# Kernel optimization log

Measured on AMD Instinct MI355X. Metric: run time of the kernel, lower is better.

Reference implementation:

```python
import jax, jax.numpy as jnp
import numpy as np

EPS = 1e-06
H = 25  # num heads


def _rmsnorm(x, w, eps=EPS):
    # normalize over last dim in float32, as in the torch module
    xf = x.astype(jnp.float32)
    var = jnp.mean(xf * xf, axis=-1, keepdims=True)
    return (w * (xf * jax.lax.rsqrt(var + eps))).astype(x.dtype)


def setup_inputs() -> dict:
    key = jax.random.key(0)
    ks = jax.random.split(key, 4)
    B, N, C = 8, 1025, 3200
    x = jax.random.normal(ks[0], (B, N, C), dtype=jnp.float32)
    qkv_w = jax.random.normal(ks[1], (C, 3 * C), dtype=jnp.float32) * (C ** -0.5)
    qkv_b = jnp.zeros((3 * C,), dtype=jnp.float32)
    q_norm_w = jnp.ones((C,), dtype=jnp.float32)
    k_norm_w = jnp.ones((C,), dtype=jnp.float32)
    proj_w = jax.random.normal(ks[2], (C, C), dtype=jnp.float32) * (C ** -0.5)
    proj_b = jnp.zeros((C,), dtype=jnp.float32)
    return {"x": x, "qkv_w": qkv_w, "qkv_b": qkv_b, "q_norm_w": q_norm_w,
            "k_norm_w": k_norm_w, "proj_w": proj_w, "proj_b": proj_b}


def reference(x, qkv_w, qkv_b, q_norm_w, k_norm_w, proj_w, proj_b):
    B, N, C = x.shape
    D = C // H
    scale = D ** -0.5
    qkv = x @ qkv_w + qkv_b                      # [B, N, 3C]
    q, k, v = jnp.split(qkv, 3, axis=-1)         # each [B, N, C]
    # QK RMSNorm is over the FULL embed_dim (heads flattened), per source.
    q = _rmsnorm(q, q_norm_w)
    k = _rmsnorm(k, k_norm_w)
    q = q.reshape(B, N, H, D)
    k = k.reshape(B, N, H, D)
    v = v.reshape(B, N, H, D)
    attn = jnp.einsum('bqhd,bkhd->bhqk', q * scale, k)   # [B, H, N, N]
    attn = jax.nn.softmax(attn, axis=-1)
    out = jnp.einsum('bhqk,bkhd->bqhd', attn, v).reshape(B, N, C)
    return out @ proj_w + proj_b
```

## Files before the change

kernel.cpp:

```cpp
#include <hip/hip_runtime.h>
#include <hip/hip_bf16.h>
#include <math.h>

#define B_ 8
#define N_ 1025
#define C_ 3200
#define H_ 25
#define D_ 128
#define M_ (B_ * N_)
#define C3_ (3 * C_)

typedef unsigned short u16;
typedef unsigned int u32;
typedef short bf16x8 __attribute__((ext_vector_type(8)));
typedef float f32x4 __attribute__((ext_vector_type(4)));

__device__ inline void load_lds16(const void* g, void* s) {
    __builtin_amdgcn_global_load_lds(
        (const __attribute__((address_space(1))) void*)g,
        (__attribute__((address_space(3))) void*)s, 16, 0, 0);
}

__device__ inline void split_pair(float x0, float x1, u32& hpk, u32& lpk) {
    __hip_bfloat162 h2 = __float22bfloat162_rn(float2{x0, x1});
    union { __hip_bfloat162 b; u32 u; } cv; cv.b = h2;
    u32 h = cv.u;
    float hf0 = __uint_as_float(h << 16);
    float hf1 = __uint_as_float(h & 0xFFFF0000u);
    __hip_bfloat162 l2 = __float22bfloat162_rn(float2{x0 - hf0, x1 - hf1});
    union { __hip_bfloat162 b; u32 u; } cl; cl.b = l2;
    hpk = h; lpk = cl.u;
}

__device__ inline void split1(float x, u16& h, u16& l) {
    union { __hip_bfloat16 b; u16 u; } ch, cl;
    ch.b = __float2bfloat16(x);
    float hf = __uint_as_float(((u32)ch.u) << 16);
    cl.b = __float2bfloat16(x - hf);
    h = ch.u; l = cl.u;
}

__global__ __launch_bounds__(256) void convert_tsplit(
    const float* __restrict__ in, u16* __restrict__ hi, u16* __restrict__ lo,
    int K, int Nn, int strideN)
{
    __shared__ float T[32][33];
    const int tid = threadIdx.x;
    const int nb = blockIdx.x * 32, kb = blockIdx.y * 32;
    #pragma unroll
    for (int p = 0; p < 4; ++p) {
        int k = p * 8 + (tid >> 5), n = tid & 31;
        T[k][n] = in[(size_t)(kb + k) * strideN + nb + n];
    }
    __syncthreads();
    const int nn = tid >> 3, k0 = (tid & 7) * 4;
    u32 h0, l0, h1, l1;
    split_pair(T[k0][nn], T[k0 + 1][nn], h0, l0);
    split_pair(T[k0 + 2][nn], T[k0 + 3][nn], h1, l1);
    size_t o = (size_t)(nb + nn) * K + kb + k0;
    *(uint2*)&hi[o] = make_uint2(h0, h1);
    *(uint2*)&lo[o] = make_uint2(l0, l1);
}

__global__ __launch_bounds__(256) void gemm_asplit(
    const float* __restrict__ A,
    const u16* __restrict__ Bh, const u16* __restrict__ Bl,
    const float* __restrict__ bias, float* __restrict__ Cc,
    int M, int N, int ldc)
{
    __shared__ u16 As_h[2][512][8];
    __shared__ u16 As_l[2][512][8];
    __shared__ u16 Bs_h[2][512][8];
    __shared__ u16 Bs_l[2][512][8];

    const int tid  = threadIdx.x;
    const int lane = tid & 63;
    const int w    = tid >> 6;
    const int wm   = w & 1, wn = w >> 1;
    const int lr = lane & 15, lg = lane >> 4;

    const int gX   = gridDim.x;
    const int nwg  = gX * gridDim.y;
    const int orig = blockIdx.y * gX + blockIdx.x;
    const int q8 = nwg >> 3, r8 = nwg & 7;
    const int xcd = orig & 7, oi = orig >> 3;
    const int wg = (xcd < r8 ? xcd * (q8 + 1)
                             : r8 * (q8 + 1) + (xcd - r8) * q8) + oi;
    const int rowBase = (wg / gX) * 128;
    const int colBase = (wg % gX) * 128;

    const int brow = tid & 127, bkc = tid >> 7;
    const size_t boff0 = (size_t)(colBase + brow) * C_ + bkc * 8;
    const size_t boff1 = (size_t)(colBase + brow) * C_ + (bkc + 2) * 8;
    const int ldsA = (w * 64) * 8;
    const int ldsB = (256 + w * 64) * 8;

    const int arow = tid >> 1;
    const int akh  = (tid & 1) * 16;
    const int kc0  = akh >> 3;
    int gr0 = rowBase + arow; if (gr0 >= M) gr0 = M - 1;
    const float* aptr = A + (size_t)gr0 * C_ + akh;

    auto STAGE_B = [&](int bb, int k0) {
        const int bo = bb * 512 * 8;
        load_lds16(Bh + boff0 + k0, (u16*)Bs_h + bo + ldsA);
        load_lds16(Bl + boff0 + k0, (u16*)Bs_l + bo + ldsA);
        load_lds16(Bh + boff1 + k0, (u16*)Bs_h + bo + ldsB);
        load_lds16(Bl + boff1 + k0, (u16*)Bs_l + bo + ldsB);
    };

    auto ASPLIT = [&](int bb, const float4& x0, const float4& x1,
                      const float4& x2, const float4& x3) {
        u32 h0,h1,h2,h3,h4,h5,h6,h7, l0,l1,l2,l3,l4,l5,l6,l7;
        split_pair(x0.x, x0.y, h0, l0); split_pair(x0.z, x0.w, h1, l1);
        split_pair(x1.x, x1.y, h2, l2); split_pair(x1.z, x1.w, h3, l3);
        split_pair(x2.x, x2.y, h4, l4); split_pair(x2.z, x2.w, h5, l5);
        split_pair(x3.x, x3.y, h6, l6); split_pair(x3.z, x3.w, h7, l7);
        *(uint4*)&As_h[bb][kc0 * 128 + arow][0]       = make_uint4(h0,h1,h2,h3);
        *(uint4*)&As_h[bb][(kc0 + 1) * 128 + arow][0] = make_uint4(h4,h5,h6,h7);
        *(uint4*)&As_l[bb][kc0 * 128 + arow][0]       = make_uint4(l0,l1,l2,l3);
        *(uint4*)&As_l[bb][(kc0 + 1) * 128 + arow][0] = make_uint4(l4,l5,l6,l7);
    };

    f32x4 acc[4][4] = {};
    float4 a0, a1, a2, a3;

    {
        float4 p0 = *(const float4*)(aptr + 0);
        float4 p1 = *(const float4*)(aptr + 4);
        float4 p2 = *(const float4*)(aptr + 8);
        float4 p3 = *(const float4*)(aptr + 12);
        ASPLIT(0, p0, p1, p2, p3);
    }
    STAGE_B(0, 0);
    {
        const float* ap = aptr + 32;
        a0 = *(const float4*)(ap + 0);
        a1 = *(const float4*)(ap + 4);
        a2 = *(const float4*)(ap + 8);
        a3 = *(const float4*)(ap + 12);
    }
    asm volatile("s_waitcnt vmcnt(0) lgkmcnt(0)" ::: "memory");
    __builtin_amdgcn_s_barrier();
    asm volatile("" ::: "memory");

    int cur = 0;
    for (int k0 = 0; k0 < C_; k0 += 32) {
        if (k0 + 32 < C_) {
            STAGE_B(cur ^ 1, k0 + 32);
            ASPLIT(cur ^ 1, a0, a1, a2, a3);
            if (k0 + 64 < C_) {
                const float* ap = aptr + k0 + 64;
                a0 = *(const float4*)(ap + 0);
                a1 = *(const float4*)(ap + 4);
                a2 = *(const float4*)(ap + 8);
                a3 = *(const float4*)(ap + 12);
            }
            asm volatile("s_waitcnt vmcnt(8)" ::: "memory");
        } else {
            asm volatile("s_waitcnt vmcnt(0)" ::: "memory");
        }
        asm volatile("s_waitcnt lgkmcnt(0)" ::: "memory");
        __builtin_amdgcn_s_barrier();
        asm volatile("" ::: "memory");

        bf16x8 ah[4], al[4], bh[4], bl[4];
        #pragma unroll
        for (int i = 0; i < 4; ++i) {
            ah[i] = *(const bf16x8*)&As_h[cur][lg * 128 + wm * 64 + i * 16 + lr][0];
            al[i] = *(const bf16x8*)&As_l[cur][lg * 128 + wm * 64 + i * 16 + lr][0];
            bh[i] = *(const bf16x8*)&Bs_h[cur][lg * 128 + wn * 64 + i * 16 + lr][0];
            bl[i] = *(const bf16x8*)&Bs_l[cur][lg * 128 + wn * 64 + i * 16 + lr][0];
        }
        #pragma unroll
        for (int j = 0; j < 4; ++j)
            #pragma unroll
            for (int i = 0; i < 4; ++i)
                acc[i][j] = __builtin_amdgcn_mfma_f32_16x16x32_bf16(
                    ah[i], bh[j], acc[i][j], 0, 0, 0);
        #pragma unroll
        for (int j = 0; j < 4; ++j)
            #pragma unroll
            for (int i = 0; i < 4; ++i)
                acc[i][j] = __builtin_amdgcn_mfma_f32_16x16x32_bf16(
                    al[i], bh[j], acc[i][j], 0, 0, 0);
        #pragma unroll
        for (int j = 0; j < 4; ++j)
            #pragma unroll
            for (int i = 0; i < 4; ++i)
                acc[i][j] = __builtin_amdgcn_mfma_f32_16x16x32_bf16(
                    ah[i], bl[j], acc[i][j], 0, 0, 0);

        asm volatile("s_waitcnt lgkmcnt(0)" ::: "memory");
        __builtin_amdgcn_s_barrier();
        asm volatile("" ::: "memory");
        cur ^= 1;
    }

    #pragma unroll
    for (int i = 0; i < 4; ++i) {
        #pragma unroll
        for (int j = 0; j < 4; ++j) {
            int gc = colBase + wn * 64 + j * 16 + lr;
            float bv = bias[gc];
            #pragma unroll
            for (int r = 0; r < 4; ++r) {
                int gr = rowBase + wm * 64 + i * 16 + lg * 4 + r;
                if (gr < M) Cc[(size_t)gr * ldc + gc] = acc[i][j][r] + bv;
            }
        }
    }
}

__global__ __launch_bounds__(256) void gemm_bf16split(
    const u16* __restrict__ Ah, const u16* __restrict__ Al,
    const u16* __restrict__ Bh, const u16* __restrict__ Bl,
    const float* __restrict__ bias, float* __restrict__ Cc,
    int M, int N, int ldc)
{
    __shared__ u16 As_h[2][512][8];
    __shared__ u16 As_l[2][512][8];
    __shared__ u16 Bs_h[2][512][8];
    __shared__ u16 Bs_l[2][512][8];

    const int tid  = threadIdx.x;
    const int lane = tid & 63;
    const int w    = tid >> 6;
    const int wm   = w & 1, wn = w >> 1;
    const int lr = lane & 15, lg = lane >> 4;

    const int gX   = gridDim.x;
    const int nwg  = gX * gridDim.y;
    const int orig = blockIdx.y * gX + blockIdx.x;
    const int q8 = nwg >> 3, r8 = nwg & 7;
    const int xcd = orig & 7, oi = orig >> 3;
    const int wg = (xcd < r8 ? xcd * (q8 + 1)
                             : r8 * (q8 + 1) + (xcd - r8) * q8) + oi;
    const int rowBase = (wg / gX) * 128;
    const int colBase = (wg % gX) * 128;

    const int row = tid & 127, kc = tid >> 7;
    int ar = rowBase + row; if (ar >= M) ar = M - 1;
    const size_t aoff0 = (size_t)ar * C_ + kc * 8;
    const size_t aoff1 = (size_t)ar * C_ + (kc + 2) * 8;
    const size_t boff0 = (size_t)(colBase + row) * C_ + kc * 8;
    const size_t boff1 = (size_t)(colBase + row) * C_ + (kc + 2) * 8;
    const int ldsA = (w * 64) * 8;
    const int ldsB = (256 + w * 64) * 8;

    auto STAGE = [&](int bb, int k0) {
        const int bo = bb * 512 * 8;
        load_lds16(Ah + aoff0 + k0, (u16*)As_h + bo + ldsA);
        load_lds16(Al + aoff0 + k0, (u16*)As_l + bo + ldsA);
        load_lds16(Bh + boff0 + k0, (u16*)Bs_h + bo + ldsA);
        load_lds16(Bl + boff0 + k0, (u16*)Bs_l + bo + ldsA);
        load_lds16(Ah + aoff1 + k0, (u16*)As_h + bo + ldsB);
        load_lds16(Al + aoff1 + k0, (u16*)As_l + bo + ldsB);
        load_lds16(Bh + boff1 + k0, (u16*)Bs_h + bo + ldsB);
        load_lds16(Bl + boff1 + k0, (u16*)Bs_l + bo + ldsB);
    };

    f32x4 acc[4][4] = {};

    STAGE(0, 0);
    int cur = 0;
    for (int k0 = 0; k0 < C_; k0 += 32) {
        if (k0 + 32 < C_) {
            STAGE(cur ^ 1, k0 + 32);
            asm volatile("s_waitcnt vmcnt(8)" ::: "memory");
        } else {
            asm volatile("s_waitcnt vmcnt(0)" ::: "memory");
        }
        __builtin_amdgcn_s_barrier();
        asm volatile("" ::: "memory");

        bf16x8 ah[4], al[4], bh[4], bl[4];
        #pragma unroll
        for (int i = 0; i < 4; ++i) {
            ah[i] = *(const bf16x8*)&As_h[cur][lg * 128 + wm * 64 + i * 16 + lr][0];
            al[i] = *(const bf16x8*)&As_l[cur][lg * 128 + wm * 64 + i * 16 + lr][0];
            bh[i] = *(const bf16x8*)&Bs_h[cur][lg * 128 + wn * 64 + i * 16 + lr][0];
            bl[i] = *(const bf16x8*)&Bs_l[cur][lg * 128 + wn * 64 + i * 16 + lr][0];
        }
        #pragma unroll
        for (int j = 0; j < 4; ++j)
            #pragma unroll
            for (int i = 0; i < 4; ++i)
                acc[i][j] = __builtin_amdgcn_mfma_f32_16x16x32_bf16(
                    ah[i], bh[j], acc[i][j], 0, 0, 0);
        #pragma unroll
        for (int j = 0; j < 4; ++j)
            #pragma unroll
            for (int i = 0; i < 4; ++i)
                acc[i][j] = __builtin_amdgcn_mfma_f32_16x16x32_bf16(
                    al[i], bh[j], acc[i][j], 0, 0, 0);
        #pragma unroll
        for (int j = 0; j < 4; ++j)
            #pragma unroll
            for (int i = 0; i < 4; ++i)
                acc[i][j] = __builtin_amdgcn_mfma_f32_16x16x32_bf16(
                    ah[i], bl[j], acc[i][j], 0, 0, 0);

        asm volatile("s_waitcnt lgkmcnt(0)" ::: "memory");
        __builtin_amdgcn_s_barrier();
        asm volatile("" ::: "memory");
        cur ^= 1;
    }

    #pragma unroll
    for (int i = 0; i < 4; ++i) {
        #pragma unroll
        for (int j = 0; j < 4; ++j) {
            int gc = colBase + wn * 64 + j * 16 + lr;
            float bv = bias[gc];
            #pragma unroll
            for (int r = 0; r < 4; ++r) {
                int gr = rowBase + wm * 64 + i * 16 + lg * 4 + r;
                if (gr < M) Cc[(size_t)gr * ldc + gc] = acc[i][j][r] + bv;
            }
        }
    }
}

__global__ __launch_bounds__(256) void rmsnorm_kernel(
    float* __restrict__ qkv, const float* __restrict__ qw,
    const float* __restrict__ kw)
{
    const int row   = blockIdx.x >> 1;
    const int which = blockIdx.x & 1;
    float* p = qkv + (size_t)row * C3_ + which * C_;
    const float* w = which ? kw : qw;
    const int tid = threadIdx.x;

    float ss = 0.f;
    for (int i = tid; i < C_ / 4; i += 256) {
        float4 v = ((const float4*)p)[i];
        ss += v.x * v.x + v.y * v.y + v.z * v.z + v.w * v.w;
    }
    #pragma unroll
    for (int off = 32; off; off >>= 1) ss += __shfl_down(ss, off);

    __shared__ float wsum[4];
    __shared__ float stot;
    if ((tid & 63) == 0) wsum[tid >> 6] = ss;
    __syncthreads();
    if (tid == 0) stot = wsum[0] + wsum[1] + wsum[2] + wsum[3];
    __syncthreads();

    const float scale = rsqrtf(stot / (float)C_ + 1e-6f);
    for (int i = tid; i < C_ / 4; i += 256) {
        float4 v  = ((const float4*)p)[i];
        float4 wv = ((const float4*)w)[i];
        v.x *= scale * wv.x; v.y *= scale * wv.y;
        v.z *= scale * wv.z; v.w *= scale * wv.w;
        ((float4*)p)[i] = v;
    }
}

__global__ __launch_bounds__(256, 2) void flash_mfma(
    const float* __restrict__ qkv, u16* __restrict__ aoh, u16* __restrict__ aol)
{
    __shared__ u16 Kh[4][32][32];
    __shared__ u16 Kl[4][32][32];
    __shared__ u16 Vth[128][40];
    __shared__ u16 Vtl[128][40];
    __shared__ u16 Ph[4][16][40];
    __shared__ u16 Pl[4][16][40];

    const int b   = blockIdx.z;
    const int h   = blockIdx.y;
    const int q0  = blockIdx.x * 64;
    const int tid = threadIdx.x;
    const int lane = tid & 63;
    const int w    = tid >> 6;
    const int lr = lane & 15, lg = lane >> 4;
    const float scale = 0.088388347648318447f;

    bf16x8 qh[4], ql[4];
    {
        int qr = q0 + w * 16 + lr;
        if (qr >= N_) qr = N_ - 1;
        const float* qp = qkv + (size_t)(b * N_ + qr) * C3_ + h * D_;
        #pragma unroll
        for (int c = 0; c < 4; ++c) {
            float4 x0 = *(const float4*)(qp + c * 32 + lg * 8);
            float4 x1 = *(const float4*)(qp + c * 32 + lg * 8 + 4);
            union { u32 u[4]; bf16x8 v; } Hq, Lq;
            split_pair(x0.x * scale, x0.y * scale, Hq.u[0], Lq.u[0]);
            split_pair(x0.z * scale, x0.w * scale, Hq.u[1], Lq.u[1]);
            split_pair(x1.x * scale, x1.y * scale, Hq.u[2], Lq.u[2]);
            split_pair(x1.z * scale, x1.w * scale, Hq.u[3], Lq.u[3]);
            qh[c] = Hq.v; ql[c] = Lq.v;
        }
    }

    const float* Kbase = qkv + (size_t)b * N_ * C3_ + C_ + h * D_;
    const float* Vbase = qkv + (size_t)b * N_ * C3_ + 2 * C_ + h * D_;

    const int skr = tid >> 3;
    const int skd = (tid & 7) * 16;
    const int svk = (tid & 15) * 2;
    const int svd = (tid >> 4) * 4;

    float4 kg[4], vg[2][2];

    auto stage_load = [&](int kt) {
        int kk = kt * 32 + skr;
        if (kk < N_) {
            const float* p = Kbase + (size_t)kk * C3_ + skd;
            kg[0] = *(const float4*)(p + 0);
            kg[1] = *(const float4*)(p + 4);
            kg[2] = *(const float4*)(p + 8);
            kg[3] = *(const float4*)(p + 12);
        } else {
            kg[0] = kg[1] = kg[2] = kg[3] = make_float4(0.f, 0.f, 0.f, 0.f);
        }
        #pragma unroll
        for (int r = 0; r < 2; ++r) {
            int vk = kt * 32 + svk + r;
            if (vk < N_) {
                const float* p = Vbase + (size_t)vk * C3_ + svd;
                vg[0][r] = *(const float4*)(p);
                vg[1][r] = *(const float4*)(p + 64);
            } else {
                vg[0][r] = make_float4(0.f, 0.f, 0.f, 0.f);
                vg[1][r] = make_float4(0.f, 0.f, 0.f, 0.f);
            }
        }
    };

    auto stage_store = [&]() {
        #pragma unroll
        for (int i = 0; i < 4; ++i) {
            int d = skd + i * 4;
            int c = d >> 5, dd = d & 31;
            u32 h0, l0, h1, l1;
            split_pair(kg[i].x, kg[i].y, h0, l0);
            split_pair(kg[i].z, kg[i].w, h1, l1);
            *(uint2*)&Kh[c][skr][dd] = make_uint2(h0, h1);
            *(uint2*)&Kl[c][skr][dd] = make_uint2(l0, l1);
        }
        #pragma unroll
        for (int half = 0; half < 2; ++half) {
            float a0[4] = { vg[half][0].x, vg[half][0].y, vg[half][0].z, vg[half][0].w };
            float a1[4] = { vg[half][1].x, vg[half][1].y, vg[half][1].z, vg[half][1].w };
            #pragma unroll
            for (int i = 0; i < 4; ++i) {
                int d = svd + half * 64 + i;
                u32 hp, lp;
                split_pair(a0[i], a1[i], hp, lp);
                *(u32*)&Vth[d][svk] = hp;
                *(u32*)&Vtl[d][svk] = lp;
            }
        }
    };

    f32x4 oacc[8] = {};
    float m[4]    = { -INFINITY, -INFINITY, -INFINITY, -INFINITY };
    float lsum[4] = { 0.f, 0.f, 0.f, 0.f };

    const int nkt = (N_ + 31) / 32;
    stage_load(0);
    for (int kt = 0; kt < nkt; ++kt) {
        __syncthreads();
        stage_store();
        __syncthreads();
        if (kt + 1 < nkt) stage_load(kt + 1);

        f32x4 s0 = {}, s1 = {};
        #pragma unroll
        for (int c = 0; c < 4; ++c) {
            bf16x8 kh0 = *(const bf16x8*)&Kh[c][lr][lg * 8];
            bf16x8 kl0 = *(const bf16x8*)&Kl[c][lr][lg * 8];
            bf16x8 kh1 = *(const bf16x8*)&Kh[c][16 + lr][lg * 8];
            bf16x8 kl1 = *(const bf16x8*)&Kl[c][16 + lr][lg * 8];
            s0 = __builtin_amdgcn_mfma_f32_16x16x32_bf16(qh[c], kh0, s0, 0, 0, 0);
            s0 = __builtin_amdgcn_mfma_f32_16x16x32_bf16(ql[c], kh0, s0, 0, 0, 0);
            s0 = __builtin_amdgcn_mfma_f32_16x16x32_bf16(qh[c], kl0, s0, 0, 0, 0);
            s1 = __builtin_amdgcn_mfma_f32_16x16x32_bf16(qh[c], kh1, s1, 0, 0, 0);
            s1 = __builtin_amdgcn_mfma_f32_16x16x32_bf16(ql[c], kh1, s1, 0, 0, 0);
            s1 = __builtin_amdgcn_mfma_f32_16x16x32_bf16(qh[c], kl1, s1, 0, 0, 0);
        }

        const int kb = kt * 32;
        const bool v0 = (kb + lr) < N_;
        const bool v1 = (kb + 16 + lr) < N_;
        #pragma unroll
        for (int r = 0; r < 4; ++r) {
            if (!v0) s0[r] = -INFINITY;
            if (!v1) s1[r] = -INFINITY;
        }

        #pragma unroll
        for (int r = 0; r < 4; ++r) {
            float mt = fmaxf(s0[r], s1[r]);
            mt = fmaxf(mt, __shfl_xor(mt, 1));
            mt = fmaxf(mt, __shfl_xor(mt, 2));
            mt = fmaxf(mt, __shfl_xor(mt, 4));
            mt = fmaxf(mt, __shfl_xor(mt, 8));
            float mn = fmaxf(m[r], mt);
            float al = __expf(m[r] - mn);
            m[r] = mn;
            float p0 = __expf(s0[r] - mn);
            float p1 = __expf(s1[r] - mn);
            float ls = p0 + p1;
            ls += __shfl_xor(ls, 1);
            ls += __shfl_xor(ls, 2);
            ls += __shfl_xor(ls, 4);
            ls += __shfl_xor(ls, 8);
            lsum[r] = lsum[r] * al + ls;
            #pragma unroll
            for (int dt = 0; dt < 8; ++dt) oacc[dt][r] *= al;

            u16 hh, ll;
            split1(p0, hh, ll);
            Ph[w][lg * 4 + r][lr] = hh;
            Pl[w][lg * 4 + r][lr] = ll;
            split1(p1, hh, ll);
            Ph[w][lg * 4 + r][16 + lr] = hh;
            Pl[w][lg * 4 + r][16 + lr] = ll;
        }

        bf16x8 pah = *(const bf16x8*)&Ph[w][lr][lg * 8];
        bf16x8 pal = *(const bf16x8*)&Pl[w][lr][lg * 8];
        #pragma unroll
        for (int dt = 0; dt < 8; ++dt) {
            bf16x8 vh = *(const bf16x8*)&Vth[dt * 16 + lr][lg * 8];
            bf16x8 vl = *(const bf16x8*)&Vtl[dt * 16 + lr][lg * 8];
            oacc[dt] = __builtin_amdgcn_mfma_f32_16x16x32_bf16(pah, vh, oacc[dt], 0, 0, 0);
            oacc[dt] = __builtin_amdgcn_mfma_f32_16x16x32_bf16(pal, vh, oacc[dt], 0, 0, 0);
            oacc[dt] = __builtin_amdgcn_mfma_f32_16x16x32_bf16(pah, vl, oacc[dt], 0, 0, 0);
        }
    }

    #pragma unroll
    for (int r = 0; r < 4; ++r) {
        int q = q0 + w * 16 + lg * 4 + r;
        if (q < N_) {
            float inv = 1.f / lsum[r];
            size_t base = (size_t)(b * N_ + q) * C_ + h * D_ + lr;
            #pragma unroll
            for (int dt = 0; dt < 8; ++dt) {
                u16 hh, ll;
                split1(oacc[dt][r] * inv, hh, ll);
                aoh[base + dt * 16] = hh;
                aol[base + dt * 16] = ll;
            }
        }
    }
}

extern "C" void kernel_launch(void* const* d_in, const int* in_sizes, int n_in,
                              void* d_out, int out_size, void* d_ws, size_t ws_size,
                              hipStream_t stream)
{
    const float* x        = (const float*)d_in[0];
    const float* qkv_w    = (const float*)d_in[1];
    const float* qkv_b    = (const float*)d_in[2];
    const float* q_norm_w = (const float*)d_in[3];
    const float* k_norm_w = (const float*)d_in[4];
    const float* proj_w   = (const float*)d_in[5];
    const float* proj_b   = (const float*)d_in[6];
    float* out = (float*)d_out;

    const size_t fQ = (size_t)M_ * C3_;
    const size_t fA = (size_t)M_ * C_;
    const size_t wC = (size_t)C_ * C_;

    float* qkv = (float*)d_ws;
    u16*   R   = (u16*)(qkv + fQ);

    dim3 blk(256);

    u16* wh = R;
    u16* wl = wh + wC;
    for (int j = 0; j < 3; ++j) {
        convert_tsplit<<<dim3(C_ / 32, C_ / 32), blk, 0, stream>>>(
            qkv_w + (size_t)j * C_, wh, wl, C_, C_, C3_);
        gemm_asplit<<<dim3(C_ / 128, (M_ + 127) / 128), blk, 0, stream>>>(
            x, wh, wl, qkv_b + j * C_, qkv + (size_t)j * C_, M_, C_, C3_);
    }

    rmsnorm_kernel<<<dim3(M_ * 2), blk, 0, stream>>>(qkv, q_norm_w, k_norm_w);
    u16* aoh = R;
    u16* aol = R + fA;
    flash_mfma<<<dim3((N_ + 63) / 64, H_, B_), blk, 0, stream>>>(qkv, aoh, aol);

    u16* ph = (u16*)d_ws;
    u16* pl = ph + wC;
    convert_tsplit<<<dim3(C_ / 32, C_ / 32), blk, 0, stream>>>(
        proj_w, ph, pl, C_, C_, C_);
    gemm_bf16split<<<dim3(C_ / 128, (M_ + 127) / 128), blk, 0, stream>>>(
        aoh, aol, ph, pl, proj_b, out, M_, C_, C_);
}
```

Before: 4.507 ms.

## Reuse asplit GEMM for projection, restructure barriers, add MFMA priority

The attention kernel now writes fp32 output directly instead of pre-split bf16 hi/lo arrays. The output projection runs through the gemm_asplit kernel, which splits A on the fly, and the separate gemm_bf16split kernel is removed. In gemm_asplit, the wait and barrier move to the top of each iteration, one end-of-loop barrier is dropped, and s_setprio is raised around the MFMA block. This removes the extra bf16 split-array traffic and one sync per step, but attention now writes more bytes in fp32, and the new barrier placement risks a race on the double buffer.

```diff
diff --git a/kernel.cpp b/kernel.cpp
--- a/kernel.cpp
+++ b/kernel.cpp
@@ -140,12 +140,13 @@
         a2 = *(const float4*)(ap + 8);
         a3 = *(const float4*)(ap + 12);
     }
-    asm volatile("s_waitcnt vmcnt(0) lgkmcnt(0)" ::: "memory");
-    __builtin_amdgcn_s_barrier();
-    asm volatile("" ::: "memory");
 
     int cur = 0;
     for (int k0 = 0; k0 < C_; k0 += 32) {
+        asm volatile("s_waitcnt vmcnt(0) lgkmcnt(0)" ::: "memory");
+        __builtin_amdgcn_s_barrier();
+        asm volatile("" ::: "memory");
+
         if (k0 + 32 < C_) {
             STAGE_B(cur ^ 1, k0 + 32);
             ASPLIT(cur ^ 1, a0, a1, a2, a3);
@@ -156,13 +157,7 @@
                 a2 = *(const float4*)(ap + 8);
                 a3 = *(const float4*)(ap + 12);
             }
-            asm volatile("s_waitcnt vmcnt(8)" ::: "memory");
-        } else {
-            asm volatile("s_waitcnt vmcnt(0)" ::: "memory");
-        }
-        asm volatile("s_waitcnt lgkmcnt(0)" ::: "memory");
-        __builtin_amdgcn_s_barrier();
-        asm volatile("" ::: "memory");
+        }
 
         bf16x8 ah[4], al[4], bh[4], bl[4];
         #pragma unroll
@@ -172,6 +167,7 @@
             bh[i] = *(const bf16x8*)&Bs_h[cur][lg * 128 + wn * 64 + i * 16 + lr][0];
             bl[i] = *(const bf16x8*)&Bs_l[cur][lg * 128 + wn * 64 + i * 16 + lr][0];
         }
+        __builtin_amdgcn_s_setprio(1);
         #pragma unroll
         for (int j = 0; j < 4; ++j)
             #pragma unroll
@@ -190,120 +186,7 @@
             for (int i = 0; i < 4; ++i)
                 acc[i][j] = __builtin_amdgcn_mfma_f32_16x16x32_bf16(
                     ah[i], bl[j], acc[i][j], 0, 0, 0);
-
-        asm volatile("s_waitcnt lgkmcnt(0)" ::: "memory");
-        __builtin_amdgcn_s_barrier();
-        asm volatile("" ::: "memory");
-        cur ^= 1;
-    }
-
-    #pragma unroll
-    for (int i = 0; i < 4; ++i) {
-        #pragma unroll
-        for (int j = 0; j < 4; ++j) {
-            int gc = colBase + wn * 64 + j * 16 + lr;
-            float bv = bias[gc];
-            #pragma unroll
-            for (int r = 0; r < 4; ++r) {
-                int gr = rowBase + wm * 64 + i * 16 + lg * 4 + r;
-                if (gr < M) Cc[(size_t)gr * ldc + gc] = acc[i][j][r] + bv;
-            }
-        }
-    }
-}
-
-__global__ __launch_bounds__(256) void gemm_bf16split(
-    const u16* __restrict__ Ah, const u16* __restrict__ Al,
-    const u16* __restrict__ Bh, const u16* __restrict__ Bl,
-    const float* __restrict__ bias, float* __restrict__ Cc,
-    int M, int N, int ldc)
-{
-    __shared__ u16 As_h[2][512][8];
-    __shared__ u16 As_l[2][512][8];
-    __shared__ u16 Bs_h[2][512][8];
-    __shared__ u16 Bs_l[2][512][8];
-
-    const int tid  = threadIdx.x;
-    const int lane = tid & 63;
-    const int w    = tid >> 6;
-    const int wm   = w & 1, wn = w >> 1;
-    const int lr = lane & 15, lg = lane >> 4;
-
-    const int gX   = gridDim.x;
-    const int nwg  = gX * gridDim.y;
-    const int orig = blockIdx.y * gX + blockIdx.x;
-    const int q8 = nwg >> 3, r8 = nwg & 7;
-    const int xcd = orig & 7, oi = orig >> 3;
-    const int wg = (xcd < r8 ? xcd * (q8 + 1)
-                             : r8 * (q8 + 1) + (xcd - r8) * q8) + oi;
-    const int rowBase = (wg / gX) * 128;
-    const int colBase = (wg % gX) * 128;
-
-    const int row = tid & 127, kc = tid >> 7;
-    int ar = rowBase + row; if (ar >= M) ar = M - 1;
-    const size_t aoff0 = (size_t)ar * C_ + kc * 8;
-    const size_t aoff1 = (size_t)ar * C_ + (kc + 2) * 8;
-    const size_t boff0 = (size_t)(colBase + row) * C_ + kc * 8;
-    const size_t boff1 = (size_t)(colBase + row) * C_ + (kc + 2) * 8;
-    const int ldsA = (w * 64) * 8;
-    const int ldsB = (256 + w * 64) * 8;
-
-    auto STAGE = [&](int bb, int k0) {
-        const int bo = bb * 512 * 8;
-        load_lds16(Ah + aoff0 + k0, (u16*)As_h + bo + ldsA);
-        load_lds16(Al + aoff0 + k0, (u16*)As_l + bo + ldsA);
-        load_lds16(Bh + boff0 + k0, (u16*)Bs_h + bo + ldsA);
-        load_lds16(Bl + boff0 + k0, (u16*)Bs_l + bo + ldsA);
-        load_lds16(Ah + aoff1 + k0, (u16*)As_h + bo + ldsB);
-        load_lds16(Al + aoff1 + k0, (u16*)As_l + bo + ldsB);
-        load_lds16(Bh + boff1 + k0, (u16*)Bs_h + bo + ldsB);
-        load_lds16(Bl + boff1 + k0, (u16*)Bs_l + bo + ldsB);
-    };
-
-    f32x4 acc[4][4] = {};
-
-    STAGE(0, 0);
-    int cur = 0;
-    for (int k0 = 0; k0 < C_; k0 += 32) {
-        if (k0 + 32 < C_) {
-            STAGE(cur ^ 1, k0 + 32);
-            asm volatile("s_waitcnt vmcnt(8)" ::: "memory");
-        } else {
-            asm volatile("s_waitcnt vmcnt(0)" ::: "memory");
-        }
-        __builtin_amdgcn_s_barrier();
-        asm volatile("" ::: "memory");
-
-        bf16x8 ah[4], al[4], bh[4], bl[4];
-        #pragma unroll
-        for (int i = 0; i < 4; ++i) {
-            ah[i] = *(const bf16x8*)&As_h[cur][lg * 128 + wm * 64 + i * 16 + lr][0];
-            al[i] = *(const bf16x8*)&As_l[cur][lg * 128 + wm * 64 + i * 16 + lr][0];
-            bh[i] = *(const bf16x8*)&Bs_h[cur][lg * 128 + wn * 64 + i * 16 + lr][0];
-            bl[i] = *(const bf16x8*)&Bs_l[cur][lg * 128 + wn * 64 + i * 16 + lr][0];
-        }
-        #pragma unroll
-        for (int j = 0; j < 4; ++j)
-            #pragma unroll
-            for (int i = 0; i < 4; ++i)
-                acc[i][j] = __builtin_amdgcn_mfma_f32_16x16x32_bf16(
-                    ah[i], bh[j], acc[i][j], 0, 0, 0);
-        #pragma unroll
-        for (int j = 0; j < 4; ++j)
-            #pragma unroll
-            for (int i = 0; i < 4; ++i)
-                acc[i][j] = __builtin_amdgcn_mfma_f32_16x16x32_bf16(
-                    al[i], bh[j], acc[i][j], 0, 0, 0);
-        #pragma unroll
-        for (int j = 0; j < 4; ++j)
-            #pragma unroll
-            for (int i = 0; i < 4; ++i)
-                acc[i][j] = __builtin_amdgcn_mfma_f32_16x16x32_bf16(
-                    ah[i], bl[j], acc[i][j], 0, 0, 0);
-
-        asm volatile("s_waitcnt lgkmcnt(0)" ::: "memory");
-        __builtin_amdgcn_s_barrier();
-        asm volatile("" ::: "memory");
+        __builtin_amdgcn_s_setprio(0);
         cur ^= 1;
     }
 
@@ -358,7 +241,7 @@
 }
 
 __global__ __launch_bounds__(256, 2) void flash_mfma(
-    const float* __restrict__ qkv, u16* __restrict__ aoh, u16* __restrict__ aol)
+    const float* __restrict__ qkv, float* __restrict__ attn_out)
 {
     __shared__ u16 Kh[4][32][32];
     __shared__ u16 Kl[4][32][32];
@@ -538,14 +421,9 @@
         int q = q0 + w * 16 + lg * 4 + r;
         if (q < N_) {
             float inv = 1.f / lsum[r];
-            size_t base = (size_t)(b * N_ + q) * C_ + h * D_ + lr;
-            #pragma unroll
-            for (int dt = 0; dt < 8; ++dt) {
-                u16 hh, ll;
-                split1(oacc[dt][r] * inv, hh, ll);
-                aoh[base + dt * 16] = hh;
-                aol[base + dt * 16] = ll;
-            }
+            float* op = attn_out + (size_t)(b * N_ + q) * C_ + h * D_ + lr;
+            #pragma unroll
+            for (int dt = 0; dt < 8; ++dt) op[dt * 16] = oacc[dt][r] * inv;
         }
     }
 }
@@ -582,14 +460,13 @@
     }
 
     rmsnorm_kernel<<<dim3(M_ * 2), blk, 0, stream>>>(qkv, q_norm_w, k_norm_w);
-    u16* aoh = R;
-    u16* aol = R + fA;
-    flash_mfma<<<dim3((N_ + 63) / 64, H_, B_), blk, 0, stream>>>(qkv, aoh, aol);
+    float* attn_out = (float*)R;
+    flash_mfma<<<dim3((N_ + 63) / 64, H_, B_), blk, 0, stream>>>(qkv, attn_out);
 
     u16* ph = (u16*)d_ws;
     u16* pl = ph + wC;
     convert_tsplit<<<dim3(C_ / 32, C_ / 32), blk, 0, stream>>>(
         proj_w, ph, pl, C_, C_, C_);
-    gemm_bf16split<<<dim3(C_ / 128, (M_ + 127) / 128), blk, 0, stream>>>(
-        aoh, aol, ph, pl, proj_b, out, M_, C_, C_);
-}
+    gemm_asplit<<<dim3(C_ / 128, (M_ + 127) / 128), blk, 0, stream>>>(
+        attn_out, ph, pl, proj_b, out, M_, C_, C_);
+}
```

After: 4.322 ms. -4.1%, faster.
